# Kernel optimization log

Hardware: AMD Instinct MI355X
Metric: run time of the kernel (lower is better)

The kernel has to match this reference:

```python
import jax, jax.numpy as jnp
import numpy as np

DIM = 1024
NUM_HEADS = 16
HEAD_DIM = DIM // NUM_HEADS
SCALE = HEAD_DIM ** (-0.5)
B, N = 2, 2048


def setup_inputs() -> dict:
    key = jax.random.key(0)
    ks = jax.random.split(key, 9)
    s = DIM ** (-0.5)
    return {
        "x": jax.random.normal(ks[0], (B, N, DIM), dtype=jnp.float32),
        "Wq": jax.random.normal(ks[1], (DIM, DIM), dtype=jnp.float32) * s,
        "bq": jax.random.normal(ks[2], (DIM,), dtype=jnp.float32) * 0.01,
        "Wk": jax.random.normal(ks[3], (DIM, DIM), dtype=jnp.float32) * s,
        "bk": jax.random.normal(ks[4], (DIM,), dtype=jnp.float32) * 0.01,
        "Wv": jax.random.normal(ks[5], (DIM, DIM), dtype=jnp.float32) * s,
        "bv": jax.random.normal(ks[6], (DIM,), dtype=jnp.float32) * 0.01,
        "Wp": jax.random.normal(ks[7], (DIM, DIM), dtype=jnp.float32) * s,
        "bp": jax.random.normal(ks[8], (DIM,), dtype=jnp.float32) * 0.01,
    }


def reference(x, Wq, bq, Wk, bk, Wv, bv, Wp, bp):
    Bb, Nn, C = x.shape
    # Linear layers (torch Linear: x @ W.T + b)
    q = x @ Wq.T + bq
    k = x @ Wk.T + bk
    v = x @ Wv.T + bv
    # [B, H, N, Dh]
    q = q.reshape(Bb, Nn, NUM_HEADS, HEAD_DIM).transpose(0, 2, 1, 3) * SCALE
    k = k.reshape(Bb, Nn, NUM_HEADS, HEAD_DIM).transpose(0, 2, 1, 3)
    v = v.reshape(Bb, Nn, NUM_HEADS, HEAD_DIM).transpose(0, 2, 1, 3)
    # float32 scores (original casts q,k to float before matmul)
    attn = jnp.einsum("bhnd,bhmd->bhnm", q.astype(jnp.float32), k.astype(jnp.float32))
    attn = jax.nn.softmax(attn, axis=-1).astype(x.dtype)
    out = jnp.einsum("bhnm,bhmd->bhnd", attn, v)
    out = out.transpose(0, 2, 1, 3).reshape(Bb, Nn, C)
    return out @ Wp.T + bp
```

## Files before the change

### kernel.cpp

```cpp
#include <hip/hip_runtime.h>
#include <hip/hip_bf16.h>
#include <stdint.h>

#define SEQ   2048
#define NDIM  1024
#define NH    16
#define DH    64
#define NB    2
#define MROWS (NB*SEQ)
#define S2SCALE (0.125f * 1.44269504f)

typedef __attribute__((ext_vector_type(8))) short bf16x8;
typedef __attribute__((ext_vector_type(4))) float f32x4;


__device__ __forceinline__ unsigned short f2bf(float f) {
  union { float f; unsigned int u; } v; v.f = f;
  unsigned int u = v.u;
  return (unsigned short)((u + 0x7fffu + ((u >> 16) & 1u)) >> 16);
}

__device__ __forceinline__ float exp2fast(float x) {
#if __has_builtin(__builtin_amdgcn_exp2f)
  return __builtin_amdgcn_exp2f(x);
#else
  float r; asm volatile("v_exp_f32 %0, %1" : "=v"(r) : "v"(x)); return r;
#endif
}

__device__ __forceinline__ void drain_vmem() {
  asm volatile("s_waitcnt vmcnt(0)" ::: "memory");
  __builtin_amdgcn_sched_barrier(0);
}

__device__ __forceinline__ void gld16(const void* g, void* l) {
  __builtin_amdgcn_global_load_lds(
      (const __attribute__((address_space(1))) void*)g,
      (__attribute__((address_space(3))) void*)l,
      16, 0, 0);
}

__global__ __launch_bounds__(256) void cvt_all(
    const float* __restrict__ x,  const float* __restrict__ wq,
    const float* __restrict__ wk, const float* __restrict__ wv,
    const float* __restrict__ wp,
    unsigned short* __restrict__ xb,  unsigned short* __restrict__ wqb,
    unsigned short* __restrict__ wkb, unsigned short* __restrict__ wvb,
    unsigned short* __restrict__ wpb)
{
  int c = blockIdx.x * 256 + threadIdx.x;
  const float* s; unsigned short* d;
  if (c < (MROWS*NDIM/8)) { s = x; d = xb; }
  else {
    c -= MROWS*NDIM/8;
    int w = c >> 17; c &= (1<<17)-1;
    s = (w==0)?wq:(w==1)?wk:(w==2)?wv:wp;
    d = (w==0)?wqb:(w==1)?wkb:(w==2)?wvb:wpb;
  }
  size_t off = (size_t)c * 8;
  const float4* sp = (const float4*)(s + off);
  float4 a = sp[0], b4 = sp[1];
  unsigned int u0 = (unsigned)f2bf(a.x)  | ((unsigned)f2bf(a.y)  << 16);
  unsigned int u1 = (unsigned)f2bf(a.z)  | ((unsigned)f2bf(a.w)  << 16);
  unsigned int u2 = (unsigned)f2bf(b4.x) | ((unsigned)f2bf(b4.y) << 16);
  unsigned int u3 = (unsigned)f2bf(b4.z) | ((unsigned)f2bf(b4.w) << 16);
  uint4 o; o.x = u0; o.y = u1; o.z = u2; o.w = u3;
  *(uint4*)(d + off) = o;
}

template<int BM>
__device__ __forceinline__ void gemm_loop(
    const unsigned short* __restrict__ A0,
    const unsigned short* __restrict__ B0,
    int K, f32x4 (&acc)[BM/32][4], char* ldsA, char* ldsB)
{
  constexpr int MI   = BM/32;
  constexpr int APIT = BM/32;
  const int tid = threadIdx.x;
  const int lane = tid & 63, g = lane >> 4, l15 = lane & 15;
  const int wv = tid >> 6, wm = wv >> 1, wn = wv & 1;

  int srowA[APIT], scolA[APIT], srowB[4], scolB[4];
#pragma unroll
  for (int p = 0; p < APIT; ++p) {
    int idx = p*256 + tid;
    int row = idx >> 3, c = idx & 7;
    srowA[p] = row;
    scolA[p] = (c ^ (row & 7)) * 8;
  }
#pragma unroll
  for (int p = 0; p < 4; ++p) {
    int idx = p*256 + tid;
    int row = idx >> 3, c = idx & 7;
    srowB[p] = row;
    scolB[p] = (c ^ (row & 7)) * 8;
  }
  int offA[MI][2], offB[4][2];
#pragma unroll
  for (int f = 0; f < MI; ++f) {
    int ra = wm*(BM/2) + f*16 + l15;
#pragma unroll
    for (int kc = 0; kc < 2; ++kc)
      offA[f][kc] = ra*128 + (((kc*4 + g) ^ (ra & 7)) * 16);
  }
#pragma unroll
  for (int f = 0; f < 4; ++f) {
    int rb = wn*64 + f*16 + l15;
#pragma unroll
    for (int kc = 0; kc < 2; ++kc)
      offB[f][kc] = rb*128 + (((kc*4 + g) ^ (rb & 7)) * 16);
  }

  for (int k0 = 0; k0 < K; k0 += 64) {
#pragma unroll
    for (int p = 0; p < APIT; ++p)
      gld16(A0 + (size_t)srowA[p]*K + k0 + scolA[p], ldsA + p*4096 + wv*1024);
#pragma unroll
    for (int p = 0; p < 4; ++p)
      gld16(B0 + (size_t)srowB[p]*K + k0 + scolB[p], ldsB + p*4096 + wv*1024);
    drain_vmem();
    __syncthreads();
    bf16x8 af[MI][2], bfr[4][2];
#pragma unroll
    for (int f = 0; f < MI; ++f)
#pragma unroll
      for (int kc = 0; kc < 2; ++kc) af[f][kc] = *(const bf16x8*)(ldsA + offA[f][kc]);
#pragma unroll
    for (int f = 0; f < 4; ++f)
#pragma unroll
      for (int kc = 0; kc < 2; ++kc) bfr[f][kc] = *(const bf16x8*)(ldsB + offB[f][kc]);
#pragma unroll
    for (int kc = 0; kc < 2; ++kc)
#pragma unroll
      for (int i = 0; i < MI; ++i)
#pragma unroll
        for (int j = 0; j < 4; ++j)
          acc[i][j] = __builtin_amdgcn_mfma_f32_16x16x32_bf16(af[i][kc], bfr[j][kc], acc[i][j], 0, 0, 0);
    __syncthreads();
  }
}

__global__ __launch_bounds__(256, 3) void gemm_qkv(
    const unsigned short* __restrict__ xb,
    const unsigned short* __restrict__ wqb, const unsigned short* __restrict__ wkb,
    const unsigned short* __restrict__ wvb,
    const float* __restrict__ bq, const float* __restrict__ bk, const float* __restrict__ bv,
    unsigned short* __restrict__ qb, unsigned short* __restrict__ kb,
    unsigned short* __restrict__ vtb)
{
  __shared__ __align__(16) char lds[32768];
  const int z = blockIdx.z;
  const unsigned short* W = (z==0)?wqb:(z==1)?wkb:wvb;
  const float* bias = (z==0)?bq:(z==1)?bk:bv;
  const int n0 = blockIdx.x * 128, m0 = blockIdx.y * 128;

  f32x4 acc[4][4];
#pragma unroll
  for (int i = 0; i < 4; ++i)
#pragma unroll
    for (int j = 0; j < 4; ++j) acc[i][j] = (f32x4){0.f, 0.f, 0.f, 0.f};

  gemm_loop<128>(xb + (size_t)m0*NDIM, W + (size_t)n0*NDIM, NDIM, acc, lds, lds + 16384);

  const int lane = threadIdx.x & 63, g = lane >> 4, l15 = lane & 15;
  const int wvx = threadIdx.x >> 6, wm = wvx >> 1, wn = wvx & 1;

  if (z < 2) {
    unsigned short* out = (z==0) ? qb : kb;
    const float sc = (z==0) ? S2SCALE : 1.0f;
#pragma unroll
    for (int i = 0; i < 4; ++i)
#pragma unroll
      for (int j = 0; j < 4; ++j) {
        int col = n0 + wn*64 + j*16 + l15;
        float bb = bias[col];
#pragma unroll
        for (int r = 0; r < 4; ++r) {
          int row = m0 + wm*64 + i*16 + g*4 + r;
          out[(size_t)row*NDIM + col] = f2bf((acc[i][j][r] + bb) * sc);
        }
      }
  } else {
#pragma unroll
    for (int i = 0; i < 4; ++i)
#pragma unroll
      for (int j = 0; j < 4; ++j) {
        int col = n0 + wn*64 + j*16 + l15;
        float bb = bias[col];
        int row0 = m0 + wm*64 + i*16 + g*4;
        int b_ = row0 >> 11, n_ = row0 & (SEQ-1);
        unsigned long long pk =
            (unsigned long long)f2bf(acc[i][j][0] + bb)
          | ((unsigned long long)f2bf(acc[i][j][1] + bb) << 16)
          | ((unsigned long long)f2bf(acc[i][j][2] + bb) << 32)
          | ((unsigned long long)f2bf(acc[i][j][3] + bb) << 48);
        *(unsigned long long*)(vtb + ((size_t)(b_*NDIM + col))*SEQ + n_) = pk;
      }
  }
}

__global__ __launch_bounds__(256, 2) void attn_fwd(
    const unsigned short* __restrict__ qb, const unsigned short* __restrict__ kb,
    const unsigned short* __restrict__ vtb, unsigned short* __restrict__ ob)
{
  __shared__ __align__(16) char lds[49152];
  const int tid = threadIdx.x, lane = tid & 63, g = lane >> 4, l15 = lane & 15;
  const int wvx = tid >> 6;
  char* Pw = lds + 32768 + wvx*4096;
  const int bh = blockIdx.y, b_ = bh >> 4, h = bh & 15;
  const int qbase = blockIdx.x*128 + wvx*32;

  int srow[2], scol[2];
#pragma unroll
  for (int p = 0; p < 2; ++p) {
    int idx = p*256 + tid;
    int row = idx >> 3, c = idx & 7;
    srow[p] = row;
    scol[p] = (c ^ (row & 7)) * 8;
  }

  bf16x8 qf[2][2];
#pragma unroll
  for (int fn = 0; fn < 2; ++fn) {
    size_t row = (size_t)(b_*SEQ + qbase + fn*16 + l15);
#pragma unroll
    for (int kc = 0; kc < 2; ++kc)
      qf[fn][kc] = *(const bf16x8*)(qb + row*NDIM + h*DH + kc*32 + g*8);
  }

  float m2[2]   = {-3.0e38f, -3.0e38f};
  float lacc[2] = {0.f, 0.f};
  f32x4 o_[2][4];
#pragma unroll
  for (int fn = 0; fn < 2; ++fn)
#pragma unroll
    for (int fd = 0; fd < 4; ++fd) o_[fn][fd] = (f32x4){0.f, 0.f, 0.f, 0.f};

#pragma unroll
  for (int p = 0; p < 2; ++p) {
    gld16(kb  + ((size_t)(b_*SEQ + srow[p]))*NDIM + h*DH + scol[p],
          lds + p*4096 + wvx*1024);
    gld16(vtb + ((size_t)(b_*NDIM + h*DH + srow[p]))*SEQ + scol[p],
          lds + 8192 + p*4096 + wvx*1024);
  }
  drain_vmem();
  __syncthreads();

  int cur = 0;
  for (int t = 0; t < SEQ/64; ++t) {
    if (t < SEQ/64 - 1) {
      const int k0n = (t+1)*64;
      char* Kd = lds + (cur^1)*16384;
#pragma unroll
      for (int p = 0; p < 2; ++p) {
        gld16(kb  + ((size_t)(b_*SEQ + k0n + srow[p]))*NDIM + h*DH + scol[p],
              Kd + p*4096 + wvx*1024);
        gld16(vtb + ((size_t)(b_*NDIM + h*DH + srow[p]))*SEQ + k0n + scol[p],
              Kd + 8192 + p*4096 + wvx*1024);
      }
    }
    char* Ks = lds + cur*16384;
    char* Vs = Ks + 8192;

    bf16x8 kf[4][2];
#pragma unroll
    for (int fm = 0; fm < 4; ++fm)
#pragma unroll
      for (int kc = 0; kc < 2; ++kc) {
        int row = fm*16 + l15;
        kf[fm][kc] = *(const bf16x8*)(Ks + row*128 + (((kc*4+g) ^ (row & 7))*16));
      }

    f32x4 st[2][4];
#pragma unroll
    for (int fn = 0; fn < 2; ++fn)
#pragma unroll
      for (int fm = 0; fm < 4; ++fm) st[fn][fm] = (f32x4){0.f, 0.f, 0.f, 0.f};
#pragma unroll
    for (int kc = 0; kc < 2; ++kc)
#pragma unroll
      for (int fn = 0; fn < 2; ++fn)
#pragma unroll
        for (int fm = 0; fm < 4; ++fm)
          st[fn][fm] = __builtin_amdgcn_mfma_f32_16x16x32_bf16(kf[fm][kc], qf[fn][kc], st[fn][fm], 0, 0, 0);

#pragma unroll
    for (int fn = 0; fn < 2; ++fn) {
      float tmax = -3.0e38f;
#pragma unroll
      for (int fm = 0; fm < 4; ++fm)
#pragma unroll
        for (int r = 0; r < 4; ++r)
          tmax = fmaxf(tmax, st[fn][fm][r]);
      tmax = fmaxf(tmax, __shfl_xor(tmax, 16));
      tmax = fmaxf(tmax, __shfl_xor(tmax, 32));
      if (__any(tmax > m2[fn])) {
        float mnew  = fmaxf(m2[fn], tmax);
        float alpha = exp2fast(m2[fn] - mnew);
        m2[fn] = mnew;
        lacc[fn] *= alpha;
#pragma unroll
        for (int fd = 0; fd < 4; ++fd)
#pragma unroll
          for (int r = 0; r < 4; ++r) o_[fn][fd][r] *= alpha;
      }
      const int prow = fn*16 + l15;
#pragma unroll
      for (int fm = 0; fm < 4; ++fm) {
        float p0 = exp2fast(st[fn][fm][0] - m2[fn]);
        float p1 = exp2fast(st[fn][fm][1] - m2[fn]);
        float p2 = exp2fast(st[fn][fm][2] - m2[fn]);
        float p3 = exp2fast(st[fn][fm][3] - m2[fn]);
        lacc[fn] += (p0 + p1) + (p2 + p3);
        unsigned long long pk =
            (unsigned long long)f2bf(p0)
          | ((unsigned long long)f2bf(p1) << 16)
          | ((unsigned long long)f2bf(p2) << 32)
          | ((unsigned long long)f2bf(p3) << 48);
        *(unsigned long long*)(Pw + prow*128 + (((fm*2 + (g>>1)) ^ (prow & 7))*16) + (g & 1)*8) = pk;
      }
    }

    bf16x8 vf[4][2];
#pragma unroll
    for (int fd = 0; fd < 4; ++fd)
#pragma unroll
      for (int ks = 0; ks < 2; ++ks) {
        int row = fd*16 + l15;
        vf[fd][ks] = *(const bf16x8*)(Vs + row*128 + (((ks*4+g) ^ (row & 7))*16));
      }
    bf16x8 pf[2][2];
#pragma unroll
    for (int fn = 0; fn < 2; ++fn)
#pragma unroll
      for (int ks = 0; ks < 2; ++ks) {
        int row = fn*16 + l15;
        pf[fn][ks] = *(const bf16x8*)(Pw + row*128 + (((ks*4+g) ^ (row & 7))*16));
      }
#pragma unroll
    for (int ks = 0; ks < 2; ++ks)
#pragma unroll
      for (int fn = 0; fn < 2; ++fn)
#pragma unroll
        for (int fd = 0; fd < 4; ++fd)
          o_[fn][fd] = __builtin_amdgcn_mfma_f32_16x16x32_bf16(vf[fd][ks], pf[fn][ks], o_[fn][fd], 0, 0, 0);

    drain_vmem();
    __syncthreads();
    cur ^= 1;
  }

#pragma unroll
  for (int fn = 0; fn < 2; ++fn) {
    float l = lacc[fn];
    l += __shfl_xor(l, 16);
    l += __shfl_xor(l, 32);
    float inv = 1.f / l;
    size_t row = (size_t)(b_*SEQ + qbase + fn*16 + l15);
#pragma unroll
    for (int fd = 0; fd < 4; ++fd) {
      unsigned long long pk =
          (unsigned long long)f2bf(o_[fn][fd][0]*inv)
        | ((unsigned long long)f2bf(o_[fn][fd][1]*inv) << 16)
        | ((unsigned long long)f2bf(o_[fn][fd][2]*inv) << 32)
        | ((unsigned long long)f2bf(o_[fn][fd][3]*inv) << 48);
      *(unsigned long long*)(ob + row*NDIM + h*DH + fd*16 + g*4) = pk;
    }
  }
}

__global__ __launch_bounds__(256, 2) void gemm_proj(
    const unsigned short* __restrict__ ob, const unsigned short* __restrict__ wpb,
    const float* __restrict__ bp, float* __restrict__ out)
{
  __shared__ __align__(16) char lds[24576];
  const int n0 = blockIdx.x * 128, m0 = blockIdx.y * 64;
  f32x4 acc[2][4];
#pragma unroll
  for (int i = 0; i < 2; ++i)
#pragma unroll
    for (int j = 0; j < 4; ++j) acc[i][j] = (f32x4){0.f, 0.f, 0.f, 0.f};

  gemm_loop<64>(ob + (size_t)m0*NDIM, wpb + (size_t)n0*NDIM, NDIM, acc, lds, lds + 8192);

  const int lane = threadIdx.x & 63, g = lane >> 4, l15 = lane & 15;
  const int wvx = threadIdx.x >> 6, wm = wvx >> 1, wn = wvx & 1;
#pragma unroll
  for (int i = 0; i < 2; ++i)
#pragma unroll
    for (int j = 0; j < 4; ++j) {
      int col = n0 + wn*64 + j*16 + l15;
      float bb = bp[col];
#pragma unroll
      for (int r = 0; r < 4; ++r) {
        int row = m0 + wm*32 + i*16 + g*4 + r;
        out[(size_t)row*NDIM + col] = acc[i][j][r] + bb;
      }
    }
}

extern "C" void kernel_launch(void* const* d_in, const int* in_sizes, int n_in,
                              void* d_out, int out_size, void* d_ws, size_t ws_size,
                              hipStream_t stream) {
  const float* x  = (const float*)d_in[0];
  const float* Wq = (const float*)d_in[1];
  const float* bq = (const float*)d_in[2];
  const float* Wk = (const float*)d_in[3];
  const float* bk = (const float*)d_in[4];
  const float* Wv = (const float*)d_in[5];
  const float* bv = (const float*)d_in[6];
  const float* Wp = (const float*)d_in[7];
  const float* bp = (const float*)d_in[8];
  float* out = (float*)d_out;

  char* ws = (char*)d_ws;
  const size_t MB = (size_t)1 << 20;
  unsigned short* xb  = (unsigned short*)(ws + 0*MB);
  unsigned short* wqb = (unsigned short*)(ws + 8*MB);
  unsigned short* wkb = (unsigned short*)(ws + 10*MB);
  unsigned short* wvb = (unsigned short*)(ws + 12*MB);
  unsigned short* wpb = (unsigned short*)(ws + 14*MB);
  unsigned short* qb  = (unsigned short*)(ws + 16*MB);
  unsigned short* kb  = (unsigned short*)(ws + 24*MB);
  unsigned short* vtb = (unsigned short*)(ws + 32*MB);
  unsigned short* ob  = (unsigned short*)(ws + 40*MB);

  hipLaunchKernelGGL(cvt_all, dim3(4096), dim3(256), 0, stream,
                     x, Wq, Wk, Wv, Wp, xb, wqb, wkb, wvb, wpb);
  hipLaunchKernelGGL(gemm_qkv, dim3(NDIM/128, MROWS/128, 3), dim3(256), 0, stream,
                     xb, wqb, wkb, wvb, bq, bk, bv, qb, kb, vtb);
  hipLaunchKernelGGL(attn_fwd, dim3(SEQ/128, NB*NH), dim3(256), 0, stream,
                     qb, kb, vtb, ob);
  hipLaunchKernelGGL(gemm_proj, dim3(NDIM/128, MROWS/64), dim3(256), 0, stream,
                     ob, wpb, bp, out);
}
```

Baseline: 198.6 us.

## Build P operand in registers via permlane swaps instead of LDS round-trip

The softmax probabilities are no longer written to a per-wave LDS scratch and read back as MFMA operands. Instead they are packed into bf16 pairs and rearranged across lanes with v_permlane32_swap and v_permlane16_swap to form the B-operand fragments directly. This removes LDS traffic and frees 16 KB of shared memory, which could allow more blocks per CU. It also wraps the MFMA loops in s_setprio and restructures the row-max reduction as a tree. The lane permutation must exactly match the MFMA operand layout, otherwise results are wrong.

```diff
diff --git a/kernel.cpp b/kernel.cpp
--- a/kernel.cpp
+++ b/kernel.cpp
@@ -26,6 +26,13 @@
 #else
   float r; asm volatile("v_exp_f32 %0, %1" : "=v"(r) : "v"(x)); return r;
 #endif
+}
+
+__device__ __forceinline__ void pl32swap(unsigned int& x, unsigned int& y) {
+  asm("v_permlane32_swap_b32 %0, %1" : "+v"(x), "+v"(y));
+}
+__device__ __forceinline__ void pl16swap(unsigned int& x, unsigned int& y) {
+  asm("v_permlane16_swap_b32 %0, %1" : "+v"(x), "+v"(y));
 }
 
 __device__ __forceinline__ void drain_vmem() {
@@ -203,10 +210,9 @@
     const unsigned short* __restrict__ qb, const unsigned short* __restrict__ kb,
     const unsigned short* __restrict__ vtb, unsigned short* __restrict__ ob)
 {
-  __shared__ __align__(16) char lds[49152];
+  __shared__ __align__(16) char lds[32768];
   const int tid = threadIdx.x, lane = tid & 63, g = lane >> 4, l15 = lane & 15;
   const int wvx = tid >> 6;
-  char* Pw = lds + 32768 + wvx*4096;
   const int bh = blockIdx.y, b_ = bh >> 4, h = bh & 15;
   const int qbase = blockIdx.x*128 + wvx*32;
 
@@ -276,6 +282,7 @@
     for (int fn = 0; fn < 2; ++fn)
 #pragma unroll
       for (int fm = 0; fm < 4; ++fm) st[fn][fm] = (f32x4){0.f, 0.f, 0.f, 0.f};
+    __builtin_amdgcn_s_setprio(1);
 #pragma unroll
     for (int kc = 0; kc < 2; ++kc)
 #pragma unroll
@@ -283,15 +290,16 @@
 #pragma unroll
         for (int fm = 0; fm < 4; ++fm)
           st[fn][fm] = __builtin_amdgcn_mfma_f32_16x16x32_bf16(kf[fm][kc], qf[fn][kc], st[fn][fm], 0, 0, 0);
-
+    __builtin_amdgcn_s_setprio(0);
+
+    bf16x8 pf[2][2];
 #pragma unroll
     for (int fn = 0; fn < 2; ++fn) {
-      float tmax = -3.0e38f;
-#pragma unroll
-      for (int fm = 0; fm < 4; ++fm)
-#pragma unroll
-        for (int r = 0; r < 4; ++r)
-          tmax = fmaxf(tmax, st[fn][fm][r]);
+      float ma = fmaxf(fmaxf(st[fn][0][0], st[fn][0][1]), fmaxf(st[fn][0][2], st[fn][0][3]));
+      float mb = fmaxf(fmaxf(st[fn][1][0], st[fn][1][1]), fmaxf(st[fn][1][2], st[fn][1][3]));
+      float mc = fmaxf(fmaxf(st[fn][2][0], st[fn][2][1]), fmaxf(st[fn][2][2], st[fn][2][3]));
+      float md = fmaxf(fmaxf(st[fn][3][0], st[fn][3][1]), fmaxf(st[fn][3][2], st[fn][3][3]));
+      float tmax = fmaxf(fmaxf(ma, mb), fmaxf(mc, md));
       tmax = fmaxf(tmax, __shfl_xor(tmax, 16));
       tmax = fmaxf(tmax, __shfl_xor(tmax, 32));
       if (__any(tmax > m2[fn])) {
@@ -304,7 +312,7 @@
 #pragma unroll
           for (int r = 0; r < 4; ++r) o_[fn][fd][r] *= alpha;
       }
-      const int prow = fn*16 + l15;
+      unsigned int w[4][2];
 #pragma unroll
       for (int fm = 0; fm < 4; ++fm) {
         float p0 = exp2fast(st[fn][fm][0] - m2[fn]);
@@ -312,12 +320,18 @@
         float p2 = exp2fast(st[fn][fm][2] - m2[fn]);
         float p3 = exp2fast(st[fn][fm][3] - m2[fn]);
         lacc[fn] += (p0 + p1) + (p2 + p3);
-        unsigned long long pk =
-            (unsigned long long)f2bf(p0)
-          | ((unsigned long long)f2bf(p1) << 16)
-          | ((unsigned long long)f2bf(p2) << 32)
-          | ((unsigned long long)f2bf(p3) << 48);
-        *(unsigned long long*)(Pw + prow*128 + (((fm*2 + (g>>1)) ^ (prow & 7))*16) + (g & 1)*8) = pk;
+        w[fm][0] = (unsigned)f2bf(p0) | ((unsigned)f2bf(p1) << 16);
+        w[fm][1] = (unsigned)f2bf(p2) | ((unsigned)f2bf(p3) << 16);
+      }
+#pragma unroll
+      for (int kc = 0; kc < 2; ++kc) {
+        unsigned int x0 = w[kc*2][0], y0 = w[kc*2+1][0];
+        pl32swap(x0, y0); pl16swap(x0, y0);
+        unsigned int x1 = w[kc*2][1], y1 = w[kc*2+1][1];
+        pl32swap(x1, y1); pl16swap(x1, y1);
+        union { unsigned int u[4]; bf16x8 v; } uu;
+        uu.u[0] = x0; uu.u[1] = x1; uu.u[2] = y0; uu.u[3] = y1;
+        pf[fn][kc] = uu.v;
       }
     }
 
@@ -329,14 +343,7 @@
         int row = fd*16 + l15;
         vf[fd][ks] = *(const bf16x8*)(Vs + row*128 + (((ks*4+g) ^ (row & 7))*16));
       }
-    bf16x8 pf[2][2];
-#pragma unroll
-    for (int fn = 0; fn < 2; ++fn)
-#pragma unroll
-      for (int ks = 0; ks < 2; ++ks) {
-        int row = fn*16 + l15;
-        pf[fn][ks] = *(const bf16x8*)(Pw + row*128 + (((ks*4+g) ^ (row & 7))*16));
-      }
+    __builtin_amdgcn_s_setprio(1);
 #pragma unroll
     for (int ks = 0; ks < 2; ++ks)
 #pragma unroll
@@ -344,6 +351,7 @@
 #pragma unroll
         for (int fd = 0; fd < 4; ++fd)
           o_[fn][fd] = __builtin_amdgcn_mfma_f32_16x16x32_bf16(vf[fd][ks], pf[fn][ks], o_[fn][fd], 0, 0, 0);
+    __builtin_amdgcn_s_setprio(0);
 
     drain_vmem();
     __syncthreads();
```

After: 202.9 us. 2.2% more time.
